# Performance work log

Measured on AMD Instinct MI355X. Metric: run time of the kernel, lower is better.

## Reference

```python
import jax, jax.numpy as jnp
import numpy as np

B, N, H, E, A, V, L = 64, 196, 512, 512, 512, 20000, 20


def setup_inputs() -> dict:
    key = jax.random.key(0)
    ks = jax.random.split(key, 16)
    s = lambda *sh: 0.02
    return {
        "encoder_outputs": jax.random.normal(ks[0], (B, N, H), dtype=jnp.float32),
        "captions": jax.random.randint(ks[1], (B, L), 0, V, dtype=jnp.int64),
        "emb": jax.random.normal(ks[2], (V, E), dtype=jnp.float32) * 0.02,
        "W_ih": jax.random.normal(ks[3], (4 * H, E + H), dtype=jnp.float32) * 0.02,
        "W_hh": jax.random.normal(ks[4], (4 * H, H), dtype=jnp.float32) * 0.02,
        "b_ih": jax.random.normal(ks[5], (4 * H,), dtype=jnp.float32) * 0.02,
        "b_hh": jax.random.normal(ks[6], (4 * H,), dtype=jnp.float32) * 0.02,
        "enc_W": jax.random.normal(ks[7], (A, H), dtype=jnp.float32) * 0.02,
        "enc_b": jax.random.normal(ks[8], (A,), dtype=jnp.float32) * 0.02,
        "dec_W": jax.random.normal(ks[9], (A, H), dtype=jnp.float32) * 0.02,
        "dec_b": jax.random.normal(ks[10], (A,), dtype=jnp.float32) * 0.02,
        "energy_W": jax.random.normal(ks[11], (1, A), dtype=jnp.float32) * 0.02,
        "energy_b": jax.random.normal(ks[12], (1,), dtype=jnp.float32) * 0.02,
        "fc_W": jax.random.normal(ks[13], (V, H), dtype=jnp.float32) * 0.02,
        "fc_b": jax.random.normal(ks[14], (V,), dtype=jnp.float32) * 0.02,
    }


def reference(encoder_outputs, captions, emb, W_ih, W_hh, b_ih, b_hh,
              enc_W, enc_b, dec_W, dec_b, energy_W, energy_b, fc_W, fc_b):
    b, max_len = captions.shape
    hid = W_hh.shape[1]
    vocab = fc_W.shape[0]
    dt = encoder_outputs.dtype

    # encoder projection is hidden-state independent: hoist out of the loop
    enc_proj = jnp.einsum('bnh,ah->bna', encoder_outputs, enc_W) + enc_b  # [B,N,A]
    # teacher forcing ratio = 1.0 => input at step t is captions[:, t-1]
    emb_seq = emb[captions[:, :-1]]                                      # [B,L-1,E]
    emb_seq = jnp.swapaxes(emb_seq, 0, 1)                                # [L-1,B,E]

    def step(carry, x_t):
        h, c = carry
        dec = h @ dec_W.T + dec_b                                        # [B,A]
        scores = jnp.tanh(enc_proj + dec[:, None, :]) @ energy_W[0] + energy_b[0]  # [B,N]
        attw = jax.nn.softmax(scores, axis=1)
        context = jnp.einsum('bn,bnh->bh', attw, encoder_outputs)        # [B,H]
        lstm_in = jnp.concatenate([x_t, context], axis=1)                # [B,E+H]
        gates = lstm_in @ W_ih.T + b_ih + h @ W_hh.T + b_hh              # [B,4H]
        i, f, g, o = jnp.split(gates, 4, axis=1)
        c_new = jax.nn.sigmoid(f) * c + jax.nn.sigmoid(i) * jnp.tanh(g)
        h_new = jax.nn.sigmoid(o) * jnp.tanh(c_new)
        out = h_new @ fc_W.T + fc_b                                      # [B,V]
        return (h_new, c_new), out

    h0 = jnp.zeros((b, hid), dtype=dt)
    c0 = jnp.zeros((b, hid), dtype=dt)
    (_, _), outs = jax.lax.scan(step, (h0, c0), emb_seq)                 # [L-1,B,V]
    outputs = jnp.concatenate(
        [jnp.zeros((b, 1, vocab), dtype=dt), jnp.swapaxes(outs, 0, 1)], axis=1)
    return outputs
```

## Files before the change

### kernel.cpp

```cpp
#include <hip/hip_runtime.h>
#include <hip/hip_bf16.h>
#include <math.h>

#define B   64
#define NN  196
#define HH  512
#define EE  512
#define AA  512
#define VV  20000
#define LL  20

typedef __attribute__((ext_vector_type(8))) short bf16x8;
typedef __attribute__((ext_vector_type(4))) float floatx4;

__device__ __forceinline__ float tanh_fast(float x) {
  float e2 = __expf(2.f * x);
  return 1.f - 2.f / (e2 + 1.f);
}
__device__ __forceinline__ float sigmoid_fast(float x) {
  return 1.f / (1.f + __expf(-x));
}
__device__ __forceinline__ float bf2f(unsigned short u) {
  return __uint_as_float(((unsigned)u) << 16);
}
__device__ __forceinline__ unsigned short f2bf(float v) {
  __hip_bfloat16 h = __float2bfloat16(v);
  return *reinterpret_cast<unsigned short*>(&h);
}

__device__ __forceinline__ unsigned ald(const unsigned* p) {
  return __hip_atomic_load(p, __ATOMIC_RELAXED, __HIP_MEMORY_SCOPE_AGENT);
}
__device__ __forceinline__ void ast(unsigned* p, unsigned v) {
  __hip_atomic_store(p, v, __ATOMIC_RELAXED, __HIP_MEMORY_SCOPE_AGENT);
}
__device__ __forceinline__ int aldi(const int* p) {
  return __hip_atomic_load(p, __ATOMIC_RELAXED, __HIP_MEMORY_SCOPE_AGENT);
}
__device__ __forceinline__ void asti(int* p, int v) {
  __hip_atomic_store(p, v, __ATOMIC_RELAXED, __HIP_MEMORY_SCOPE_AGENT);
}

__device__ __forceinline__ int ldsw(int row, int q4) {
  return (row * 4 + (q4 ^ ((row >> 1) & 3))) * 8;
}
__device__ __forceinline__ int ldsw8(int row, int q8) {
  return (row * 8 + (q8 ^ (row & 7))) * 8;
}

__global__ __launch_bounds__(256) void gemm_mfma_bt(
    const unsigned short* __restrict__ Xb, const unsigned short* __restrict__ Wb,
    const float* __restrict__ bias, float* __restrict__ C,
    int M, int N, int K, int lda, int ldC, int outMode, int gridMX) {
  __shared__ unsigned short As[128 * 32];
  __shared__ unsigned short Bs[128 * 32];
  const int tid = threadIdx.x;
  const int lane = tid & 63;
  const int l15 = lane & 15;
  const int q = lane >> 4;
  const int wv = tid >> 6;
  const int wm = (wv >> 1) * 64;
  const int wn = (wv & 1) * 64;
  int mBase, nBase;
  if (gridMX == 2) {
    const int MT = (M + 127) >> 7, NT = (N + 127) >> 7;
    int wg = blockIdx.x;
    int xcd = wg & 7, idx = wg >> 3;
    int kk = idx / MT, mi = idx - kk * MT;
    int p = kk * 8 + xcd;
    if (p >= NT) return;
    mBase = mi * 128;
    nBase = p * 128;
  } else {
    mBase = blockIdx.y * 128;
    nBase = blockIdx.x * 128;
  }

  const int c0 = tid, c1 = tid + 256;
  const int r0 = c0 >> 2, q0 = c0 & 3;
  const int r1 = c1 >> 2, q1 = c1 & 3;
  const int s0 = ldsw(r0, q0), s1 = ldsw(r1, q1);

  floatx4 zero = {0.f, 0.f, 0.f, 0.f};
  floatx4 acc[4][4];
#pragma unroll
  for (int i = 0; i < 4; ++i)
#pragma unroll
    for (int j = 0; j < 4; ++j) acc[i][j] = zero;

  for (int k0 = 0; k0 < K; k0 += 32) {
    uint4 a0 = *(const uint4*)(Xb + (size_t)(mBase + r0) * lda + k0 + q0 * 8);
    uint4 a1 = *(const uint4*)(Xb + (size_t)(mBase + r1) * lda + k0 + q1 * 8);
    uint4 b0 = *(const uint4*)(Wb + (size_t)(nBase + r0) * K + k0 + q0 * 8);
    uint4 b1 = *(const uint4*)(Wb + (size_t)(nBase + r1) * K + k0 + q1 * 8);
    __syncthreads();
    *(uint4*)&As[s0] = a0;
    *(uint4*)&As[s1] = a1;
    *(uint4*)&Bs[s0] = b0;
    *(uint4*)&Bs[s1] = b1;
    __syncthreads();
    bf16x8 af[4], bfv[4];
#pragma unroll
    for (int i = 0; i < 4; ++i)
      af[i] = *(const bf16x8*)&As[ldsw(wm + i * 16 + l15, q)];
#pragma unroll
    for (int j = 0; j < 4; ++j)
      bfv[j] = *(const bf16x8*)&Bs[ldsw(wn + j * 16 + l15, q)];
#pragma unroll
    for (int i = 0; i < 4; ++i)
#pragma unroll
      for (int j = 0; j < 4; ++j)
        acc[i][j] = __builtin_amdgcn_mfma_f32_16x16x32_bf16(af[i], bfv[j],
                                                            acc[i][j], 0, 0, 0);
  }

#pragma unroll
  for (int i = 0; i < 4; ++i) {
#pragma unroll
    for (int j = 0; j < 4; ++j) {
#pragma unroll
      for (int p = 0; p < 4; ++p) {
        int m = mBase + wm + i * 16 + q * 4 + p;
        int n = nBase + wn + j * 16 + l15;
        if (m < M && n < N) {
          float v = acc[i][j][p];
          if (bias) v += bias[n];
          if (outMode == 1) {
            size_t idx = (size_t)(m & 63) * ((size_t)LL * VV) +
                         (size_t)((m >> 6) + 1) * VV + n;
            C[idx] = v;
          } else if (outMode == 2) {
            ((unsigned short*)C)[(size_t)m * ldC + n] = f2bf(v);
          } else {
            C[(size_t)m * ldC + n] = v;
          }
        }
      }
    }
  }
}

__global__ __launch_bounds__(512) void decoder_persist(
    const unsigned short* __restrict__ enc_projb,
    const unsigned short* __restrict__ encOutb,
    const unsigned short* __restrict__ dec_Wp,
    const float* __restrict__ dec_b, const float* __restrict__ eW,
    const float* __restrict__ eb,
    const unsigned short* __restrict__ Wgi,
    const float* __restrict__ gates_all_,
    float* __restrict__ c,
    unsigned short* __restrict__ xcat2,
    unsigned short* __restrict__ hb,
    int* __restrict__ flags) {
  const int tid = threadIdx.x;
  __shared__ __align__(16) char smem[153600];
  int* fctx = flags;
  int* fh = flags + 64;

  if (blockIdx.x < 64) {
    const int b = blockIdx.x;
    unsigned short* projL = (unsigned short*)smem;
    float* hs = (float*)(smem + 131072);
    float* sdec = (float*)(smem + 133120);
    float* sw = (float*)(smem + 135168);
    float* tmp = (float*)(smem + 136192);
    float* cpR = (float*)(smem + 137216);
    const int wvv = tid >> 6, lane = tid & 63;
    float ew8[8];
#pragma unroll
    for (int j = 0; j < 8; ++j) ew8[j] = eW[lane * 8 + j];
    float eb0 = eb[0];
    float dbv = dec_b[tid];

    {
      const uint4* src = (const uint4*)(enc_projb + (size_t)b * NN * 512);
      uint4* dst = (uint4*)projL;
      for (int i = tid; i < 128 * 64; i += 512) dst[i] = src[i];
    }

    for (int s = 0; s < 19; ++s) {
      unsigned* xc32 = (unsigned*)(xcat2 + (size_t)(s & 1) * 131072);
      if (s > 0) {
        if (tid < 16) {
          while (aldi(&fh[tid]) < s) __builtin_amdgcn_s_sleep(1);
        }
        __syncthreads();
        if (tid < 256) {
          unsigned u = ald(xc32 + (b << 9) + tid);
          hs[2 * tid] = bf2f((unsigned short)(u & 0xffffu));
          hs[2 * tid + 1] = bf2f((unsigned short)(u >> 16));
        }
        __syncthreads();
        float dacc = dbv;
#pragma unroll 4
        for (int kg = 0; kg < 64; ++kg) {
          bf16x8 w8 = *(const bf16x8*)(dec_Wp + (size_t)((kg << 9) + tid) * 8);
#pragma unroll
          for (int j = 0; j < 8; ++j)
            dacc += hs[kg * 8 + j] * bf2f((unsigned short)w8[j]);
        }
        sdec[tid] = dacc;
      } else {
        sdec[tid] = dbv;
      }
      __syncthreads();

      float sd8[8];
#pragma unroll
      for (int j = 0; j < 8; ++j) sd8[j] = sdec[lane * 8 + j];
      for (int n = wvv; n < 128; n += 8) {
        bf16x8 v8 = *(const bf16x8*)&projL[n * 512 + lane * 8];
        float a = 0.f;
#pragma unroll
        for (int j = 0; j < 8; ++j)
          a += tanh_fast(bf2f((unsigned short)v8[j]) + sd8[j]) * ew8[j];
#pragma unroll
        for (int off = 32; off; off >>= 1) a += __shfl_down(a, off, 64);
        if (lane == 0) sw[n] = a + eb0;
      }
      {
        const unsigned short* epb =
            enc_projb + (size_t)b * NN * 512 + lane * 8;
        int n = 128 + wvv;
        bf16x8 v8 = *(const bf16x8*)(epb + (size_t)n * 512);
#pragma unroll 1
        while (true) {
          int n2 = n + 8;
          bf16x8 vnx = v8;
          if (n2 < NN) vnx = *(const bf16x8*)(epb + (size_t)n2 * 512);
          float a = 0.f;
#pragma unroll
          for (int j = 0; j < 8; ++j)
            a += tanh_fast(bf2f((unsigned short)v8[j]) + sd8[j]) * ew8[j];
#pragma unroll
          for (int off = 32; off; off >>= 1) a += __shfl_down(a, off, 64);
          if (lane == 0) sw[n] = a + eb0;
          v8 = vnx;
          n = n2;
          if (n >= NN) break;
        }
      }
      __syncthreads();

      float v = (tid < NN) ? sw[tid] : -1e30f;
      if (tid < 256) tmp[tid] = v;
      __syncthreads();
      for (int st = 128; st; st >>= 1) {
        if (tid < st) tmp[tid] = fmaxf(tmp[tid], tmp[tid + st]);
        __syncthreads();
      }
      float mx = tmp[0];
      __syncthreads();
      float e = (tid < NN) ? __expf(v - mx) : 0.f;
      if (tid < 256) tmp[tid] = e;
      __syncthreads();
      for (int st = 128; st; st >>= 1) {
        if (tid < st) tmp[tid] += tmp[tid + st];
        __syncthreads();
      }
      float inv = 1.f / tmp[0];
      if (tid < NN) sw[tid] = e * inv;
      __syncthreads();

      {
        const int st = tid >> 6;
        const int cg = tid & 63;
        float a[8] = {0.f, 0.f, 0.f, 0.f, 0.f, 0.f, 0.f, 0.f};
        const unsigned short* eo =
            encOutb + (size_t)b * NN * 512 + cg * 8;
        int n = st;
        bf16x8 v8 = *(const bf16x8*)(eo + (size_t)n * 512);
#pragma unroll 1
        while (true) {
          int n2 = n + 8;
          bf16x8 vnx = v8;
          if (n2 < NN) vnx = *(const bf16x8*)(eo + (size_t)n2 * 512);
          float w = sw[n];
#pragma unroll
          for (int j = 0; j < 8; ++j)
            a[j] += w * bf2f((unsigned short)v8[j]);
          v8 = vnx;
          n = n2;
          if (n >= NN) break;
        }
        floatx4 a0v = {a[0], a[1], a[2], a[3]};
        floatx4 a1v = {a[4], a[5], a[6], a[7]};
        *(floatx4*)&cpR[st * 512 + cg * 8] = a0v;
        *(floatx4*)&cpR[st * 512 + cg * 8 + 4] = a1v;
      }
      __syncthreads();
      if (tid < 256) {
        float v0 = 0.f, v1 = 0.f;
#pragma unroll
        for (int st = 0; st < 8; ++st) {
          v0 += cpR[st * 512 + 2 * tid];
          v1 += cpR[st * 512 + 2 * tid + 1];
        }
        unsigned pk = (unsigned)f2bf(v0) | ((unsigned)f2bf(v1) << 16);
        ast(xc32 + (b << 9) + 256 + tid, pk);
      }
      asm volatile("s_waitcnt vmcnt(0)" ::: "memory");
      __syncthreads();
      if (tid == 0) asti(&fctx[b], s + 1);
    }
  } else {
    const int g = blockIdx.x - 64;
    const int nBase = g * 128;
    unsigned short* As = (unsigned short*)smem;
    unsigned short* Bs = (unsigned short*)(smem + 8192);
    float(*gbuf)[132] = (float(*)[132])(smem + 24576);

    const int ar = tid >> 3, aq = tid & 7;
    const int sa = ldsw8(ar, aq);
    const int br0 = tid >> 3, bq0 = tid & 7;
    const int br1 = (tid + 512) >> 3, bq1 = tid & 7;
    const int sb0 = ldsw8(br0, bq0), sb1 = ldsw8(br1, bq1);

    const int lane = tid & 63;
    const int l15 = lane & 15;
    const int q = lane >> 4;
    const int wv = tid >> 6;
    const int wn = (wv & 3) * 32;

    for (int s = 0; s < 19; ++s) {
      unsigned* xc32 = (unsigned*)(xcat2 + (size_t)(s & 1) * 131072);
      unsigned* xn32 = (unsigned*)(xcat2 + (size_t)((s + 1) & 1) * 131072);
      const float* gx = gates_all_ + (size_t)s * 131072;
      unsigned* hb32 = (unsigned*)(hb + (size_t)s * 32768);

      if (s > 0) {
        if (tid < 16) {
          while (aldi(&fh[tid]) < s) __builtin_amdgcn_s_sleep(1);
        }
        __syncthreads();
      }

      floatx4 zero = {0.f, 0.f, 0.f, 0.f};
      floatx4 acc[4][2];
#pragma unroll
      for (int i = 0; i < 4; ++i)
#pragma unroll
        for (int j = 0; j < 2; ++j) acc[i][j] = zero;

#pragma unroll 1
      for (int ph = 0; ph < 2; ++ph) {
        if (ph == 1) {
          __syncthreads();
          if (tid < 64) {
            while (aldi(&fctx[tid]) < s + 1) __builtin_amdgcn_s_sleep(1);
          }
          __syncthreads();
        }
        const int kLo = ph * 512;
#pragma unroll 1
        for (int k0 = kLo; k0 < kLo + 512; k0 += 64) {
          const unsigned* ap = xc32 + (ar << 9) + (k0 >> 1) + aq * 4;
          unsigned au0 = ald(ap + 0);
          unsigned au1 = ald(ap + 1);
          unsigned au2 = ald(ap + 2);
          unsigned au3 = ald(ap + 3);
          uint4 b0 = *(const uint4*)(Wgi + (size_t)(nBase + br0) * 1024 + k0 +
                                     bq0 * 8);
          uint4 b1 = *(const uint4*)(Wgi + (size_t)(nBase + br1) * 1024 + k0 +
                                     bq1 * 8);
          __syncthreads();
          {
            uint4 av;
            av.x = au0; av.y = au1; av.z = au2; av.w = au3;
            *(uint4*)&As[sa] = av;
          }
          *(uint4*)&Bs[sb0] = b0;
          *(uint4*)&Bs[sb1] = b1;
          __syncthreads();
          if (tid < 256) {
#pragma unroll
            for (int ks = 0; ks < 2; ++ks) {
              bf16x8 af[4], bfv[2];
#pragma unroll
              for (int i = 0; i < 4; ++i)
                af[i] = *(const bf16x8*)&As[ldsw8(i * 16 + l15, ks * 4 + q)];
#pragma unroll
              for (int j = 0; j < 2; ++j)
                bfv[j] =
                    *(const bf16x8*)&Bs[ldsw8(wn + j * 16 + l15, ks * 4 + q)];
#pragma unroll
              for (int i = 0; i < 4; ++i)
#pragma unroll
                for (int j = 0; j < 2; ++j)
                  acc[i][j] = __builtin_amdgcn_mfma_f32_16x16x32_bf16(
                      af[i], bfv[j], acc[i][j], 0, 0, 0);
            }
          }
        }
      }

      if (tid < 256) {
#pragma unroll
        for (int i = 0; i < 4; ++i)
#pragma unroll
          for (int j = 0; j < 2; ++j)
#pragma unroll
            for (int p = 0; p < 4; ++p)
              gbuf[i * 16 + q * 4 + p][wn + j * 16 + l15] = acc[i][j][p];
      }
      __syncthreads();

#pragma unroll
      for (int it = 0; it < 2; ++it) {
        int p = it * 512 + tid;
        int bb = p >> 4, jp = p & 15;
        float4 gv0 = *(float4*)&gbuf[bb][jp * 8];
        float4 gv1 = *(float4*)&gbuf[bb][jp * 8 + 4];
        const float* gxp = gx + (size_t)bb * 2048 + nBase + jp * 8;
        float4 gx0 = *(const float4*)(gxp);
        float4 gx1 = *(const float4*)(gxp + 4);
        int jg0 = (nBase >> 2) + jp * 2;
        float cv0 = c[bb * 512 + jg0];
        float cv1 = c[bb * 512 + jg0 + 1];
        float cn0 = sigmoid_fast(gv0.y + gx0.y) * cv0 +
                    sigmoid_fast(gv0.x + gx0.x) * tanh_fast(gv0.z + gx0.z);
        float hn0 = sigmoid_fast(gv0.w + gx0.w) * tanh_fast(cn0);
        float cn1 = sigmoid_fast(gv1.y + gx1.y) * cv1 +
                    sigmoid_fast(gv1.x + gx1.x) * tanh_fast(gv1.z + gx1.z);
        float hn1 = sigmoid_fast(gv1.w + gx1.w) * tanh_fast(cn1);
        c[bb * 512 + jg0] = cn0;
        c[bb * 512 + jg0 + 1] = cn1;
        unsigned pk = (unsigned)f2bf(hn0) | ((unsigned)f2bf(hn1) << 16);
        ast(xn32 + ((bb << 10) + jg0) / 2, pk);
        hb32[((bb << 9) + jg0) / 2] = pk;
      }
      asm volatile("s_waitcnt vmcnt(0)" ::: "memory");
      __syncthreads();
      if (tid == 0) asti(&fh[g], s + 1);
    }
  }
}

#define VB_ENCOUT 2512
#define VB_WGI    4080
#define VB_WB0I   4592
#define VB_ENCW   4848
#define VB_DECW   4912
#define VB_EMB    4976
#define VB_ZOUT   5136
#define VB_CZ     5449
#define VB_XCZ    5457
#define VB_HBPAD  5489
#define VB_BSUM   5493
#define VB_TOTAL  5494

struct PrepArgs {
  const float *fc_W, *enc_out, *W_ih, *W_hh, *b_ih, *b_hh, *enc_W, *dec_W, *emb;
  const int* captions;
  unsigned short *fcWb, *encOutb, *Wgi, *Wb0i, *encWb, *dec_Wp, *embxb, *hb,
      *xcat2;
  float *bsumi, *c, *out;
  int* flags;
};

__global__ __launch_bounds__(256) void prep_all(PrepArgs A) {
  const int tid = threadIdx.x;
  const uint4 z4 = {0u, 0u, 0u, 0u};
  for (int vb = blockIdx.x; vb < VB_TOTAL; vb += gridDim.x) {
    if (vb < VB_ENCOUT) {
      int base = vb * 4096;
#pragma unroll 4
      for (int i = 0; i < 16; ++i) {
        int idx = base + i * 256 + tid;
        int r = idx >> 9, cc = idx & 511;
        float v = (r < 20000) ? A.fc_W[(size_t)r * 512 + cc] : 0.f;
        A.fcWb[idx] = f2bf(v);
      }
    } else if (vb < VB_WGI) {
      int base = (vb - VB_ENCOUT) * 4096;
#pragma unroll 4
      for (int i = 0; i < 16; ++i) {
        int idx = base + i * 256 + tid;
        A.encOutb[idx] = f2bf(A.enc_out[idx]);
      }
    } else if (vb < VB_WB0I) {
      int base = (vb - VB_WGI) * 4096;
#pragma unroll 4
      for (int i = 0; i < 16; ++i) {
        int idx = base + i * 256 + tid;
        int np = idx >> 10, k = idx & 1023;
        int row = (np & 3) * 512 + (np >> 2);
        float v = (k < 512) ? A.W_hh[(size_t)row * 512 + k]
                            : A.W_ih[(size_t)row * 1024 + 512 + (k - 512)];
        A.Wgi[idx] = f2bf(v);
      }
    } else if (vb < VB_ENCW) {
      int base = (vb - VB_WB0I) * 4096;
#pragma unroll 4
      for (int i = 0; i < 16; ++i) {
        int idx = base + i * 256 + tid;
        int np = idx >> 9, k = idx & 511;
        int row = (np & 3) * 512 + (np >> 2);
        A.Wb0i[idx] = f2bf(A.W_ih[(size_t)row * 1024 + k]);
      }
    } else if (vb < VB_DECW) {
      int base = (vb - VB_ENCW) * 4096;
#pragma unroll 4
      for (int i = 0; i < 16; ++i) {
        int idx = base + i * 256 + tid;
        A.encWb[idx] = f2bf(A.enc_W[idx]);
      }
    } else if (vb < VB_EMB) {
      int base = (vb - VB_DECW) * 4096;
#pragma unroll 4
      for (int i = 0; i < 16; ++i) {
        int idx = base + i * 256 + tid;
        int kg = idx >> 12, rem = idx & 4095;
        int a = rem >> 3, j = rem & 7;
        A.dec_Wp[idx] = f2bf(A.dec_W[(size_t)a * 512 + kg * 8 + j]);
      }
    } else if (vb < VB_ZOUT) {
      int base = (vb - VB_EMB) * 4096;
#pragma unroll 4
      for (int i = 0; i < 16; ++i) {
        int idx = base + i * 256 + tid;
        int m = idx >> 9, cc = idx & 511;
        unsigned short r = 0;
        if (m < 1216) {
          int t = m >> 6, b = m & 63;
          int cap = A.captions[b * LL + t];
          r = f2bf(A.emb[(size_t)cap * 512 + cc]);
        }
        A.embxb[idx] = r;
      }
    } else if (vb < VB_CZ) {
      int u0 = (vb - VB_ZOUT) * 1024;
      floatx4 zf = {0.f, 0.f, 0.f, 0.f};
#pragma unroll
      for (int i = 0; i < 4; ++i) {
        int u = u0 + i * 256 + tid;
        if (u < 320000) {
          int b = u / 5000, v4 = u - b * 5000;
          *(floatx4*)(A.out + (size_t)b * ((size_t)LL * VV) + v4 * 4) = zf;
        }
      }
    } else if (vb < VB_XCZ) {
      int u0 = (vb - VB_CZ) * 1024;
      floatx4 zf = {0.f, 0.f, 0.f, 0.f};
#pragma unroll
      for (int i = 0; i < 4; ++i) {
        int u = u0 + i * 256 + tid;
        *(floatx4*)(A.c + (size_t)u * 4) = zf;
      }
    } else if (vb < VB_HBPAD) {
      int u0 = (vb - VB_XCZ) * 1024;
#pragma unroll
      for (int i = 0; i < 4; ++i) {
        int u = u0 + i * 256 + tid;
        ((uint4*)A.xcat2)[u] = z4;
      }
    } else if (vb < VB_BSUM) {
      int u0 = (vb - VB_HBPAD) * 1024;
      uint4* hp = (uint4*)(A.hb + (size_t)1216 * 512);
#pragma unroll
      for (int i = 0; i < 4; ++i) {
        int u = u0 + i * 256 + tid;
        hp[u] = z4;
      }
    } else {
#pragma unroll
      for (int i = 0; i < 8; ++i) {
        int e = i * 256 + tid;
        int row = (e & 3) * 512 + (e >> 2);
        A.bsumi[e] = A.b_ih[row] + A.b_hh[row];
        if (e < 80) A.flags[e] = 0;
      }
    }
  }
}

extern "C" void kernel_launch(void* const* d_in, const int* in_sizes, int n_in,
                              void* d_out, int out_size, void* d_ws, size_t ws_size,
                              hipStream_t stream) {
  const float* enc_out  = (const float*)d_in[0];
  const int*   captions = (const int*)d_in[1];
  const float* emb      = (const float*)d_in[2];
  const float* W_ih     = (const float*)d_in[3];
  const float* W_hh     = (const float*)d_in[4];
  const float* b_ih     = (const float*)d_in[5];
  const float* b_hh     = (const float*)d_in[6];
  const float* enc_W    = (const float*)d_in[7];
  const float* enc_b    = (const float*)d_in[8];
  const float* dec_W    = (const float*)d_in[9];
  const float* dec_b    = (const float*)d_in[10];
  const float* energy_W = (const float*)d_in[11];
  const float* energy_b = (const float*)d_in[12];
  const float* fc_W     = (const float*)d_in[13];
  const float* fc_b     = (const float*)d_in[14];
  float* out = (float*)d_out;

  float* ws = (float*)d_ws;
  float* c          = ws;
  float* gates_all  = c + 32768;
  float* bsumi      = gates_all + (size_t)19 * 131072;
  int*   flags      = (int*)(bsumi + 2048);
  unsigned short* enc_projb = (unsigned short*)(flags + 80);
  unsigned short* fcWb    = enc_projb + (size_t)12544 * 512;
  unsigned short* encWb   = fcWb + (size_t)20096 * 512;
  unsigned short* encOutb = encWb + (size_t)512 * 512;
  unsigned short* Wb0i    = encOutb + (size_t)12544 * 512;
  unsigned short* Wgi     = Wb0i + (size_t)2048 * 512;
  unsigned short* dec_Wp  = Wgi + (size_t)2048 * 1024;
  unsigned short* embxb   = dec_Wp + (size_t)512 * 512;
  unsigned short* hb      = embxb + (size_t)1280 * 512;
  unsigned short* xcat2   = hb + (size_t)1280 * 512;

  PrepArgs pa;
  pa.fc_W = fc_W;     pa.enc_out = enc_out; pa.W_ih = W_ih;  pa.W_hh = W_hh;
  pa.b_ih = b_ih;     pa.b_hh = b_hh;       pa.enc_W = enc_W;
  pa.dec_W = dec_W;   pa.emb = emb;         pa.captions = captions;
  pa.fcWb = fcWb;     pa.encOutb = encOutb; pa.Wgi = Wgi;    pa.Wb0i = Wb0i;
  pa.encWb = encWb;   pa.dec_Wp = dec_Wp;   pa.embxb = embxb;
  pa.hb = hb;         pa.xcat2 = xcat2;     pa.bsumi = bsumi;
  pa.c = c;           pa.out = out;         pa.flags = flags;
  prep_all<<<2560, 256, 0, stream>>>(pa);

  gemm_mfma_bt<<<dim3(16, 10), 256, 0, stream>>>(
      embxb, Wb0i, bsumi, gates_all, 1216, 2048, 512, 512, 2048, 0, 0);

  gemm_mfma_bt<<<dim3(4, 98), 256, 0, stream>>>(
      encOutb, encWb, enc_b, (float*)enc_projb, 12544, 512, 512, 512, 512, 2, 0);

  decoder_persist<<<80, 512, 0, stream>>>(
      enc_projb, encOutb, dec_Wp, dec_b, energy_W, energy_b, Wgi, gates_all,
      c, xcat2, hb, flags);

  gemm_mfma_bt<<<1600, 256, 0, stream>>>(
      hb, fcWb, fc_b, out, 1216, 20000, 512, 512, 0, 1, 2);
}
```

Before: 1.334 ms.

## Split persistent LSTM gate GEMM across 32 blocks with larger K chunks

The persistent decoder now uses 32 gate blocks of 64 columns each instead of 16 blocks of 128, so the grid grows from 80 to 96 blocks and the flag count changes to match. Each gate block stages 256-wide K chunks, with 64-bit atomic loads and a 32-way swizzled LDS layout, so the K loop has fewer barrier rounds. The attention blocks' decoder projection is split into two accumulators to expose more ILP. This aims to shorten the serial per-step critical path, at the cost of more blocks spinning on flags and more LDS use per block.

Result: faster. 1.276 ms (-4.4%).

```diff
diff --git a/kernel.cpp b/kernel.cpp
--- a/kernel.cpp
+++ b/kernel.cpp
@@ -31,6 +31,9 @@
 __device__ __forceinline__ unsigned ald(const unsigned* p) {
   return __hip_atomic_load(p, __ATOMIC_RELAXED, __HIP_MEMORY_SCOPE_AGENT);
 }
+__device__ __forceinline__ unsigned long long ald64(const unsigned long long* p) {
+  return __hip_atomic_load(p, __ATOMIC_RELAXED, __HIP_MEMORY_SCOPE_AGENT);
+}
 __device__ __forceinline__ void ast(unsigned* p, unsigned v) {
   __hip_atomic_store(p, v, __ATOMIC_RELAXED, __HIP_MEMORY_SCOPE_AGENT);
 }
@@ -44,8 +47,8 @@
 __device__ __forceinline__ int ldsw(int row, int q4) {
   return (row * 4 + (q4 ^ ((row >> 1) & 3))) * 8;
 }
-__device__ __forceinline__ int ldsw8(int row, int q8) {
-  return (row * 8 + (q8 ^ (row & 7))) * 8;
+__device__ __forceinline__ int ldsw32(int row, int q32) {
+  return (row * 32 + (q32 ^ (row & 31))) * 8;
 }
 
 __global__ __launch_bounds__(256) void gemm_mfma_bt(
@@ -181,7 +184,7 @@
     for (int s = 0; s < 19; ++s) {
       unsigned* xc32 = (unsigned*)(xcat2 + (size_t)(s & 1) * 131072);
       if (s > 0) {
-        if (tid < 16) {
+        if (tid < 32) {
           while (aldi(&fh[tid]) < s) __builtin_amdgcn_s_sleep(1);
         }
         __syncthreads();
@@ -191,15 +194,19 @@
           hs[2 * tid + 1] = bf2f((unsigned short)(u >> 16));
         }
         __syncthreads();
-        float dacc = dbv;
-#pragma unroll 4
-        for (int kg = 0; kg < 64; ++kg) {
-          bf16x8 w8 = *(const bf16x8*)(dec_Wp + (size_t)((kg << 9) + tid) * 8);
-#pragma unroll
-          for (int j = 0; j < 8; ++j)
-            dacc += hs[kg * 8 + j] * bf2f((unsigned short)w8[j]);
-        }
-        sdec[tid] = dacc;
+        float d0 = dbv, d1 = 0.f;
+#pragma unroll 2
+        for (int kg = 0; kg < 64; kg += 2) {
+          bf16x8 wa = *(const bf16x8*)(dec_Wp + (size_t)((kg << 9) + tid) * 8);
+          bf16x8 wb =
+              *(const bf16x8*)(dec_Wp + (size_t)(((kg + 1) << 9) + tid) * 8);
+#pragma unroll
+          for (int j = 0; j < 8; ++j) {
+            d0 += hs[kg * 8 + j] * bf2f((unsigned short)wa[j]);
+            d1 += hs[(kg + 1) * 8 + j] * bf2f((unsigned short)wb[j]);
+          }
+        }
+        sdec[tid] = d0 + d1;
       } else {
         sdec[tid] = dbv;
       }
@@ -305,42 +312,44 @@
     }
   } else {
     const int g = blockIdx.x - 64;
-    const int nBase = g * 128;
+    const int nBase = g * 64;
     unsigned short* As = (unsigned short*)smem;
-    unsigned short* Bs = (unsigned short*)(smem + 8192);
-    float(*gbuf)[132] = (float(*)[132])(smem + 24576);
-
-    const int ar = tid >> 3, aq = tid & 7;
-    const int sa = ldsw8(ar, aq);
-    const int br0 = tid >> 3, bq0 = tid & 7;
-    const int br1 = (tid + 512) >> 3, bq1 = tid & 7;
-    const int sb0 = ldsw8(br0, bq0), sb1 = ldsw8(br1, bq1);
+    unsigned short* Bs = (unsigned short*)(smem + 32768);
+    float(*gbuf)[68] = (float(*)[68])(smem + 65536);
+
+    int cr[4], cq[4], cs[4];
+#pragma unroll
+    for (int i = 0; i < 4; ++i) {
+      int ci = tid + i * 512;
+      cr[i] = ci >> 5;
+      cq[i] = ci & 31;
+      cs[i] = ldsw32(cr[i], cq[i]);
+    }
 
     const int lane = tid & 63;
     const int l15 = lane & 15;
     const int q = lane >> 4;
     const int wv = tid >> 6;
-    const int wn = (wv & 3) * 32;
+    const int wn = (wv & 3) * 16;
 
     for (int s = 0; s < 19; ++s) {
-      unsigned* xc32 = (unsigned*)(xcat2 + (size_t)(s & 1) * 131072);
+      const unsigned long long* xc64 =
+          (const unsigned long long*)(xcat2 + (size_t)(s & 1) * 131072);
       unsigned* xn32 = (unsigned*)(xcat2 + (size_t)((s + 1) & 1) * 131072);
       const float* gx = gates_all_ + (size_t)s * 131072;
       unsigned* hb32 = (unsigned*)(hb + (size_t)s * 32768);
 
       if (s > 0) {
-        if (tid < 16) {
+        if (tid < 32) {
           while (aldi(&fh[tid]) < s) __builtin_amdgcn_s_sleep(1);
         }
         __syncthreads();
       }
 
       floatx4 zero = {0.f, 0.f, 0.f, 0.f};
-      floatx4 acc[4][2];
-#pragma unroll
-      for (int i = 0; i < 4; ++i)
-#pragma unroll
-        for (int j = 0; j < 2; ++j) acc[i][j] = zero;
+      floatx4 acc[4];
+#pragma unroll
+      for (int i = 0; i < 4; ++i) acc[i] = zero;
 
 #pragma unroll 1
       for (int ph = 0; ph < 2; ++ph) {
@@ -351,64 +360,55 @@
           }
           __syncthreads();
         }
-        const int kLo = ph * 512;
 #pragma unroll 1
-        for (int k0 = kLo; k0 < kLo + 512; k0 += 64) {
-          const unsigned* ap = xc32 + (ar << 9) + (k0 >> 1) + aq * 4;
-          unsigned au0 = ald(ap + 0);
-          unsigned au1 = ald(ap + 1);
-          unsigned au2 = ald(ap + 2);
-          unsigned au3 = ald(ap + 3);
-          uint4 b0 = *(const uint4*)(Wgi + (size_t)(nBase + br0) * 1024 + k0 +
-                                     bq0 * 8);
-          uint4 b1 = *(const uint4*)(Wgi + (size_t)(nBase + br1) * 1024 + k0 +
-                                     bq1 * 8);
+        for (int kc = 0; kc < 2; ++kc) {
+          const int kcB = ph * 512 + kc * 256;
+          unsigned long long a64[8];
+          uint4 bv[4];
+#pragma unroll
+          for (int i = 0; i < 4; ++i) {
+            const unsigned long long* ap =
+                xc64 + (size_t)cr[i] * 256 + (kcB >> 2) + cq[i] * 2;
+            a64[2 * i] = ald64(ap);
+            a64[2 * i + 1] = ald64(ap + 1);
+            bv[i] = *(const uint4*)(Wgi + (size_t)(nBase + cr[i]) * 1024 +
+                                    kcB + cq[i] * 8);
+          }
           __syncthreads();
-          {
-            uint4 av;
-            av.x = au0; av.y = au1; av.z = au2; av.w = au3;
-            *(uint4*)&As[sa] = av;
+#pragma unroll
+          for (int i = 0; i < 4; ++i) {
+            *(unsigned long long*)&As[cs[i]] = a64[2 * i];
+            *(unsigned long long*)&As[cs[i] + 4] = a64[2 * i + 1];
+            *(uint4*)&Bs[cs[i]] = bv[i];
           }
-          *(uint4*)&Bs[sb0] = b0;
-          *(uint4*)&Bs[sb1] = b1;
           __syncthreads();
-          if (tid < 256) {
-#pragma unroll
-            for (int ks = 0; ks < 2; ++ks) {
-              bf16x8 af[4], bfv[2];
-#pragma unroll
-              for (int i = 0; i < 4; ++i)
-                af[i] = *(const bf16x8*)&As[ldsw8(i * 16 + l15, ks * 4 + q)];
-#pragma unroll
-              for (int j = 0; j < 2; ++j)
-                bfv[j] =
-                    *(const bf16x8*)&Bs[ldsw8(wn + j * 16 + l15, ks * 4 + q)];
-#pragma unroll
-              for (int i = 0; i < 4; ++i)
-#pragma unroll
-                for (int j = 0; j < 2; ++j)
-                  acc[i][j] = __builtin_amdgcn_mfma_f32_16x16x32_bf16(
-                      af[i], bfv[j], acc[i][j], 0, 0, 0);
+          if (wv < 4) {
+#pragma unroll
+            for (int k0s = 0; k0s < 8; ++k0s) {
+              bf16x8 bfv = *(const bf16x8*)&Bs[ldsw32(wn + l15, k0s * 4 + q)];
+#pragma unroll
+              for (int i = 0; i < 4; ++i) {
+                bf16x8 af =
+                    *(const bf16x8*)&As[ldsw32(i * 16 + l15, k0s * 4 + q)];
+                acc[i] = __builtin_amdgcn_mfma_f32_16x16x32_bf16(af, bfv,
+                                                                 acc[i], 0, 0, 0);
+              }
             }
           }
         }
       }
 
-      if (tid < 256) {
+      if (wv < 4) {
 #pragma unroll
         for (int i = 0; i < 4; ++i)
 #pragma unroll
-          for (int j = 0; j < 2; ++j)
-#pragma unroll
-            for (int p = 0; p < 4; ++p)
-              gbuf[i * 16 + q * 4 + p][wn + j * 16 + l15] = acc[i][j][p];
-      }
-      __syncthreads();
-
-#pragma unroll
-      for (int it = 0; it < 2; ++it) {
-        int p = it * 512 + tid;
-        int bb = p >> 4, jp = p & 15;
+          for (int p = 0; p < 4; ++p)
+            gbuf[i * 16 + q * 4 + p][wn + l15] = acc[i][p];
+      }
+      __syncthreads();
+
+      {
+        int bb = tid >> 3, jp = tid & 7;
         float4 gv0 = *(float4*)&gbuf[bb][jp * 8];
         float4 gv1 = *(float4*)&gbuf[bb][jp * 8 + 4];
         const float* gxp = gx + (size_t)bb * 2048 + nBase + jp * 8;
@@ -426,8 +426,8 @@
         c[bb * 512 + jg0] = cn0;
         c[bb * 512 + jg0 + 1] = cn1;
         unsigned pk = (unsigned)f2bf(hn0) | ((unsigned)f2bf(hn1) << 16);
-        ast(xn32 + ((bb << 10) + jg0) / 2, pk);
-        hb32[((bb << 9) + jg0) / 2] = pk;
+        ast(xn32 + (((bb << 10) + jg0) >> 1), pk);
+        hb32[((bb << 9) + jg0) >> 1] = pk;
       }
       asm volatile("s_waitcnt vmcnt(0)" ::: "memory");
       __syncthreads();
@@ -568,7 +568,7 @@
         int e = i * 256 + tid;
         int row = (e & 3) * 512 + (e >> 2);
         A.bsumi[e] = A.b_ih[row] + A.b_hh[row];
-        if (e < 80) A.flags[e] = 0;
+        if (e < 96) A.flags[e] = 0;
       }
     }
   }
@@ -599,7 +599,7 @@
   float* gates_all  = c + 32768;
   float* bsumi      = gates_all + (size_t)19 * 131072;
   int*   flags      = (int*)(bsumi + 2048);
-  unsigned short* enc_projb = (unsigned short*)(flags + 80);
+  unsigned short* enc_projb = (unsigned short*)(flags + 96);
   unsigned short* fcWb    = enc_projb + (size_t)12544 * 512;
   unsigned short* encWb   = fcWb + (size_t)20096 * 512;
   unsigned short* encOutb = encWb + (size_t)512 * 512;
@@ -626,7 +626,7 @@
   gemm_mfma_bt<<<dim3(4, 98), 256, 0, stream>>>(
       encOutb, encWb, enc_b, (float*)enc_projb, 12544, 512, 512, 512, 512, 2, 0);
 
-  decoder_persist<<<80, 512, 0, stream>>>(
+  decoder_persist<<<96, 512, 0, stream>>>(
       enc_projb, encOutb, dec_Wp, dec_b, energy_W, energy_b, Wgi, gates_all,
       c, xcat2, hb, flags);
 
```
